# Optimization experiments

Hardware: AMD Instinct MI355X
Metric: run time of the kernel (lower is better)

## Reference

```python
import jax, jax.numpy as jnp
import numpy as np

D_MODEL = 1024
NUM_HEADS = 16
HEAD_DIM = D_MODEL // NUM_HEADS  # 64
D_FF = 4096
EPS = 1e-5


def layer_norm(x, gamma, beta):
    mu = jnp.mean(x, axis=-1, keepdims=True)
    var = jnp.mean((x - mu) ** 2, axis=-1, keepdims=True)
    return (x - mu) * jax.lax.rsqrt(var + EPS) * gamma + beta


def apply_rope(t):
    # t: [B, H, S, head_dim]; interleaved-pair rotation as in RoPE.apply_rope
    S, d = t.shape[-2], t.shape[-1]
    inv_freq = 1.0 / (10000.0 ** (jnp.arange(0, d, 2, dtype=jnp.float32) / d))  # [d/2]
    angles = jnp.arange(S, dtype=jnp.float32)[:, None] * inv_freq[None, :]      # [S, d/2]
    sin, cos = jnp.sin(angles), jnp.cos(angles)
    tp = t.reshape(*t.shape[:-1], d // 2, 2)  # pairs of adjacent elements
    t0, t1 = tp[..., 0], tp[..., 1]
    rot = jnp.stack([t0 * cos - t1 * sin, t0 * sin + t1 * cos], axis=-1)
    return rot.reshape(t.shape)


def setup_inputs() -> dict:
    key = jax.random.key(0)
    ks = jax.random.split(key, 18)
    s = 0.02
    d, f = D_MODEL, D_FF
    return {
        "x": jax.random.normal(ks[0], (2, 2048, d), dtype=jnp.float32),
        "Wq": jax.random.normal(ks[1], (d, d), dtype=jnp.float32) * s,
        "bq": jnp.zeros((d,), jnp.float32),
        "Wk": jax.random.normal(ks[2], (d, d), dtype=jnp.float32) * s,
        "bk": jnp.zeros((d,), jnp.float32),
        "Wv": jax.random.normal(ks[3], (d, d), dtype=jnp.float32) * s,
        "bv": jnp.zeros((d,), jnp.float32),
        "Wo": jax.random.normal(ks[4], (d, d), dtype=jnp.float32) * s,
        "bo": jnp.zeros((d,), jnp.float32),
        "W1": jax.random.normal(ks[5], (d, f), dtype=jnp.float32) * s,
        "b1": jnp.zeros((f,), jnp.float32),
        "W2": jax.random.normal(ks[6], (f, d), dtype=jnp.float32) * s,
        "b2": jnp.zeros((d,), jnp.float32),
        "g1": jnp.ones((d,), jnp.float32),
        "beta1": jnp.zeros((d,), jnp.float32),
        "g2": jnp.ones((d,), jnp.float32),
        "beta2": jnp.zeros((d,), jnp.float32),
    }


def reference(x, Wq, bq, Wk, bk, Wv, bv, Wo, bo, W1, b1, W2, b2, g1, beta1, g2, beta2):
    B, S, d = x.shape
    H, hd = NUM_HEADS, HEAD_DIM
    x_norm = layer_norm(x, g1, beta1)
    q = (x_norm @ Wq + bq).reshape(B, S, H, hd).transpose(0, 2, 1, 3)  # [B,H,S,hd]
    k = (x_norm @ Wk + bk).reshape(B, S, H, hd).transpose(0, 2, 1, 3)
    v = (x_norm @ Wv + bv).reshape(B, S, H, hd).transpose(0, 2, 1, 3)
    q = apply_rope(q)
    k = apply_rope(k)
    q = q * (1.0 / jnp.sqrt(jnp.float32(hd)))
    scores = jnp.einsum("bhqd,bhkd->bhqk", q, k)  # [B,H,S,S]
    attn = jax.nn.softmax(scores, axis=-1)
    out = jnp.einsum("bhqk,bhkd->bhqd", attn, v)
    out = out.transpose(0, 2, 1, 3).reshape(B, S, d)
    attn_out = out @ Wo + bo
    x = x + attn_out  # dropout p=0 (eval)
    x_norm2 = layer_norm(x, g2, beta2)
    ffn = jax.nn.relu(x_norm2 @ W1 + b1) @ W2 + b2
    return x + ffn
```

## Files before the change

### kernel.cpp

```cpp
#include <hip/hip_runtime.h>

typedef unsigned short bf16_t;
typedef short short8 __attribute__((ext_vector_type(8)));
typedef float f32x4 __attribute__((ext_vector_type(4)));
typedef float f32x16 __attribute__((ext_vector_type(16)));
typedef unsigned int u32x4 __attribute__((ext_vector_type(4)));

static __device__ __forceinline__ unsigned short f2bf(float f) {
  unsigned int u = __float_as_uint(f);
  unsigned int r = (u + 0x7FFFu + ((u >> 16) & 1u)) >> 16;
  return (unsigned short)r;
}
static __device__ __forceinline__ float bf2f(unsigned short u) {
  return __uint_as_float((unsigned int)u << 16);
}
static __device__ __forceinline__ unsigned int cvt_pk_bf16(float lo, float hi) {
  unsigned int r;
  asm("v_cvt_pk_bf16_f32 %0, %1, %2" : "=v"(r) : "v"(lo), "v"(hi));
  return r;
}
static __device__ __forceinline__ void pl32swap(unsigned int& a, unsigned int& b) {
  asm("v_permlane32_swap_b32 %0, %1" : "+v"(a), "+v"(b));
}

__device__ __forceinline__ void gload_lds16(const void* g, void* l) {
  __builtin_amdgcn_global_load_lds((const __attribute__((address_space(1))) void*)g,
                                   (__attribute__((address_space(3))) void*)l,
                                   16, 0, 0);
}

__global__ __launch_bounds__(256) void prep_kernel(
    const float* __restrict__ Wq, const float* __restrict__ Wk,
    const float* __restrict__ Wv, const float* __restrict__ Wo,
    const float* __restrict__ W1, const float* __restrict__ W2,
    const float* __restrict__ x, const float* __restrict__ g1,
    const float* __restrict__ be1,
    bf16_t* __restrict__ WqkvT, bf16_t* __restrict__ W1T,
    bf16_t* __restrict__ W2T, bf16_t* __restrict__ xnb) {
  __shared__ float tile[32][33];
  const int bid = blockIdx.x;
  if (bid < 12288) {
    const float* src;
    bf16_t* dst;
    int rows, cols, bx, by;
    if (bid < 4096) {
      const int z = bid >> 10, r = bid & 1023;
      src = (z == 0) ? Wq : (z == 1) ? Wk : (z == 2) ? Wv : Wo;
      dst = WqkvT + (size_t)z * 1048576;
      rows = 1024; cols = 1024;
      bx = (r & 31) * 32; by = (r >> 5) * 32;
    } else if (bid < 8192) {
      const int r = bid - 4096;
      src = W1; dst = W1T; rows = 1024; cols = 4096;
      bx = (r & 127) * 32; by = (r >> 7) * 32;
    } else {
      const int r = bid - 8192;
      src = W2; dst = W2T; rows = 4096; cols = 1024;
      bx = (r & 31) * 32; by = (r >> 5) * 32;
    }
    const int tx = threadIdx.x & 31, ty = threadIdx.x >> 5;
#pragma unroll
    for (int i = 0; i < 32; i += 8)
      tile[ty + i][tx] = src[(size_t)(by + ty + i) * cols + (bx + tx)];
    __syncthreads();
#pragma unroll
    for (int i = 0; i < 32; i += 8)
      dst[(size_t)(bx + ty + i) * rows + (by + tx)] = f2bf(tile[tx][ty + i]);
  } else {
    const int row = bid - 12288;
    const int tid = threadIdx.x;
    const float4 v = reinterpret_cast<const float4*>(x + (size_t)row * 1024)[tid];
    float s = v.x + v.y + v.z + v.w;
    float ss = v.x * v.x + v.y * v.y + v.z * v.z + v.w * v.w;
#pragma unroll
    for (int off = 32; off; off >>= 1) {
      s += __shfl_xor(s, off, 64);
      ss += __shfl_xor(ss, off, 64);
    }
    float* red = &tile[0][0];
    const int wave = tid >> 6, lane = tid & 63;
    if (lane == 0) { red[wave] = s; red[4 + wave] = ss; }
    __syncthreads();
    const float mu = (red[0] + red[1] + red[2] + red[3]) * (1.f / 1024.f);
    const float ms = (red[4] + red[5] + red[6] + red[7]) * (1.f / 1024.f);
    const float rstd = rsqrtf(ms - mu * mu + 1e-5f);
    const float4 gg = reinterpret_cast<const float4*>(g1)[tid];
    const float4 bb = reinterpret_cast<const float4*>(be1)[tid];
    bf16_t* o = xnb + (size_t)row * 1024 + tid * 4;
    o[0] = f2bf((v.x - mu) * rstd * gg.x + bb.x);
    o[1] = f2bf((v.y - mu) * rstd * gg.y + bb.y);
    o[2] = f2bf((v.z - mu) * rstd * gg.z + bb.z);
    o[3] = f2bf((v.w - mu) * rstd * gg.w + bb.w);
  }
}

__global__ __launch_bounds__(256) void ln2_combine(const bf16_t* __restrict__ p,
                                                   const float* __restrict__ x,
                                                   const float* __restrict__ bo,
                                                   const float* __restrict__ g,
                                                   const float* __restrict__ be,
                                                   float* __restrict__ x2,
                                                   bf16_t* __restrict__ xn) {
  const int row = blockIdx.x;
  const int tid = threadIdx.x;
  const float4 xv = reinterpret_cast<const float4*>(x + (size_t)row * 1024)[tid];
  const float4 bb = reinterpret_cast<const float4*>(bo)[tid];
  float4 v = {bb.x + xv.x, bb.y + xv.y, bb.z + xv.z, bb.w + xv.w};
#pragma unroll
  for (int z = 0; z < 4; ++z) {
    const ushort4 a = reinterpret_cast<const ushort4*>(p + (size_t)z * 4194304 + (size_t)row * 1024)[tid];
    v.x += bf2f(a.x); v.y += bf2f(a.y); v.z += bf2f(a.z); v.w += bf2f(a.w);
  }
  reinterpret_cast<float4*>(x2 + (size_t)row * 1024)[tid] = v;
  float s = v.x + v.y + v.z + v.w;
  float ss = v.x * v.x + v.y * v.y + v.z * v.z + v.w * v.w;
#pragma unroll
  for (int off = 32; off; off >>= 1) {
    s += __shfl_xor(s, off, 64);
    ss += __shfl_xor(ss, off, 64);
  }
  __shared__ float red[8];
  const int wave = tid >> 6, lane = tid & 63;
  if (lane == 0) { red[wave] = s; red[4 + wave] = ss; }
  __syncthreads();
  const float mu = (red[0] + red[1] + red[2] + red[3]) * (1.f / 1024.f);
  const float ms = (red[4] + red[5] + red[6] + red[7]) * (1.f / 1024.f);
  const float rstd = rsqrtf(ms - mu * mu + 1e-5f);
  const float4 gg = reinterpret_cast<const float4*>(g)[tid];
  const float4 eb = reinterpret_cast<const float4*>(be)[tid];
  bf16_t* o = xn + (size_t)row * 1024 + tid * 4;
  o[0] = f2bf((v.x - mu) * rstd * gg.x + eb.x);
  o[1] = f2bf((v.y - mu) * rstd * gg.y + eb.y);
  o[2] = f2bf((v.z - mu) * rstd * gg.z + eb.z);
  o[3] = f2bf((v.w - mu) * rstd * gg.w + eb.w);
}

__global__ __launch_bounds__(256) void ffn_combine(const bf16_t* __restrict__ p0,
                                                   const bf16_t* __restrict__ p2,
                                                   const float* __restrict__ x2,
                                                   const float* __restrict__ b2,
                                                   float* __restrict__ out) {
  const int row = blockIdx.x;
  const int tid = threadIdx.x;
  const ushort4 a0 = reinterpret_cast<const ushort4*>(p0 + (size_t)row * 1024)[tid];
  const ushort4 a1 = reinterpret_cast<const ushort4*>(p0 + 4194304 + (size_t)row * 1024)[tid];
  const ushort4 a2 = reinterpret_cast<const ushort4*>(p2 + (size_t)row * 1024)[tid];
  const float4 xv = reinterpret_cast<const float4*>(x2 + (size_t)row * 1024)[tid];
  const float4 bb = reinterpret_cast<const float4*>(b2)[tid];
  float4 v;
  v.x = bf2f(a0.x) + bf2f(a1.x) + bf2f(a2.x) + bb.x + xv.x;
  v.y = bf2f(a0.y) + bf2f(a1.y) + bf2f(a2.y) + bb.y + xv.y;
  v.z = bf2f(a0.z) + bf2f(a1.z) + bf2f(a2.z) + bb.z + xv.z;
  v.w = bf2f(a0.w) + bf2f(a1.w) + bf2f(a2.w) + bb.w + xv.w;
  reinterpret_cast<float4*>(out + (size_t)row * 1024)[tid] = v;
}

__global__ __launch_bounds__(256) void rope_bf16(bf16_t* __restrict__ q,
                                                 bf16_t* __restrict__ k) {
  const int id = blockIdx.x * 256 + threadIdx.x;
  const int i = id & 31;
  const int s = (id >> 5) & 2047;
  const int bh = id >> 16;
  const float inv = exp2f((float)i * -0.41524101186f);
  float sn, cs;
  sincosf((float)s * inv, &sn, &cs);
  const size_t base = ((size_t)bh * 2048 + s) * 64 + 2 * i;
  unsigned int qp = *(unsigned int*)&q[base];
  unsigned int kp = *(unsigned int*)&k[base];
  const float q0 = bf2f(qp & 0xffff), q1 = bf2f(qp >> 16);
  const float k0 = bf2f(kp & 0xffff), k1 = bf2f(kp >> 16);
  const float qs = 0.18033688f;
  const unsigned int qo =
      (unsigned int)f2bf((q0 * cs - q1 * sn) * qs) |
      ((unsigned int)f2bf((q0 * sn + q1 * cs) * qs) << 16);
  const unsigned int ko =
      (unsigned int)f2bf(k0 * cs - k1 * sn) |
      ((unsigned int)f2bf(k0 * sn + k1 * cs) << 16);
  *(unsigned int*)&q[base] = qo;
  *(unsigned int*)&k[base] = ko;
}

__global__ __launch_bounds__(256) void vtrans(const bf16_t* __restrict__ v,
                                              bf16_t* __restrict__ vt) {
  __shared__ bf16_t tile[32][33];
  const int bh = blockIdx.x;
  const int s0 = blockIdx.y * 32;
  const int d0 = blockIdx.z * 32;
  const int tx = threadIdx.x & 31, ty = threadIdx.x >> 5;
  const size_t base = (size_t)bh * (2048 * 64);
#pragma unroll
  for (int i = 0; i < 32; i += 8)
    tile[ty + i][tx] = v[base + (size_t)(s0 + ty + i) * 64 + d0 + tx];
  __syncthreads();
#pragma unroll
  for (int i = 0; i < 32; i += 8)
    vt[base + (size_t)(d0 + ty + i) * 2048 + s0 + tx] = tile[tx][ty + i];
}

__global__ __launch_bounds__(256, 2) void attn6(const bf16_t* __restrict__ qb,
                                                const bf16_t* __restrict__ kb,
                                                const bf16_t* __restrict__ vt,
                                                bf16_t* __restrict__ out) {
  const int bh = blockIdx.x;
  const int tid = threadIdx.x, wave = tid >> 6, lane = tid & 63;
  const int l31 = lane & 31, hi = lane >> 5;
  const int q0 = blockIdx.y * 128 + wave * 32;
  const size_t kvb = (size_t)bh * (2048 * 64);

  __shared__ __align__(16) bf16_t Ks[2][2][4096];
  __shared__ __align__(16) bf16_t Vs[2][2][4096];

  short8 qf[4];
#pragma unroll
  for (int st = 0; st < 4; ++st)
    qf[st] = *(const short8*)&qb[kvb + (size_t)(q0 + l31) * 64 + st * 16 + hi * 8];

  int kidx[2][4];
  int vidx[2][2][2];
#pragma unroll
  for (int st = 0; st < 4; ++st) {
    const int R0 = l31, R1 = 32 + l31;
    kidx[0][st] = (R0 * 8 + (((st << 1) | hi) ^ (R0 & 7))) * 8;
    kidx[1][st] = (R1 * 8 + (((st << 1) | hi) ^ (R1 & 7))) * 8;
  }
#pragma unroll
  for (int f = 0; f < 2; ++f)
#pragma unroll
    for (int ks = 0; ks < 2; ++ks) {
      const int R0 = l31, R1 = 32 + l31;
      vidx[0][f][ks] = (R0 * 8 + (((f << 2) | (ks << 1) | hi) ^ (R0 & 7))) * 8;
      vidx[1][f][ks] = (R1 * 8 + (((f << 2) | (ks << 1) | hi) ^ (R1 & 7))) * 8;
    }

  short8 vones;
#pragma unroll
  for (int j = 0; j < 8; ++j) vones[j] = (short)0x3F80;

  f32x16 acc0 = {}, acc1 = {}, lacc = {};
  const f32x16 fz = {};

#define STAGE(DST, T0)                                                                     \
  {                                                                                        \
    _Pragma("unroll") for (int sub = 0; sub < 2; ++sub) {                                  \
      _Pragma("unroll") for (int j = 0; j < 2; ++j) {                                      \
        const int s = wave * 128 + j * 64 + lane;                                          \
        const int r = s >> 3;                                                              \
        const int c = (s & 7) ^ (r & 7);                                                   \
        gload_lds16(kb + kvb + (size_t)((T0) + sub * 64 + r) * 64 + c * 8,                 \
                    &Ks[DST][sub][(size_t)s * 8]);                                         \
        gload_lds16(vt + kvb + (size_t)r * 2048 + (T0) + sub * 64 + c * 8,                 \
                    &Vs[DST][sub][(size_t)s * 8]);                                         \
      }                                                                                    \
    }                                                                                      \
  }

#define QK(BUF, SUB, P0, P1)                                                               \
  {                                                                                        \
    short8 kfa[4], kfb[4];                                                                 \
    _Pragma("unroll") for (int st = 0; st < 4; ++st) {                                     \
      kfa[st] = *(const short8*)&Ks[BUF][SUB][kidx[0][st]];                                \
      kfb[st] = *(const short8*)&Ks[BUF][SUB][kidx[1][st]];                                \
    }                                                                                      \
    __builtin_amdgcn_s_setprio(1);                                                         \
    P0 = __builtin_amdgcn_mfma_f32_32x32x16_bf16(kfa[0], qf[0], fz, 0, 0, 0);              \
    P1 = __builtin_amdgcn_mfma_f32_32x32x16_bf16(kfb[0], qf[0], fz, 0, 0, 0);              \
    _Pragma("unroll") for (int st = 1; st < 4; ++st) {                                     \
      P0 = __builtin_amdgcn_mfma_f32_32x32x16_bf16(kfa[st], qf[st], P0, 0, 0, 0);          \
      P1 = __builtin_amdgcn_mfma_f32_32x32x16_bf16(kfb[st], qf[st], P1, 0, 0, 0);          \
    }                                                                                      \
    __builtin_amdgcn_s_setprio(0);                                                         \
  }

#define SMPV(BUF, SUB, P0, P1)                                                             \
  {                                                                                        \
    _Pragma("unroll") for (int f = 0; f < 2; ++f) {                                        \
      f32x16& p = f ? P1 : P0;                                                             \
      float e[16];                                                                         \
      _Pragma("unroll") for (int r = 0; r < 16; ++r) e[r] = exp2f(p[r]);                   \
      unsigned int a0 = cvt_pk_bf16(e[0], e[1]), b0 = cvt_pk_bf16(e[4], e[5]);             \
      unsigned int a1 = cvt_pk_bf16(e[2], e[3]), b1 = cvt_pk_bf16(e[6], e[7]);             \
      unsigned int a2 = cvt_pk_bf16(e[8], e[9]), b2 = cvt_pk_bf16(e[12], e[13]);           \
      unsigned int a3 = cvt_pk_bf16(e[10], e[11]), b3 = cvt_pk_bf16(e[14], e[15]);         \
      pl32swap(a0, b0);                                                                    \
      pl32swap(a1, b1);                                                                    \
      pl32swap(a2, b2);                                                                    \
      pl32swap(a3, b3);                                                                    \
      const u32x4 w0 = {a0, a1, b0, b1};                                                   \
      const u32x4 w1 = {a2, a3, b2, b3};                                                   \
      const short8 pf0 = __builtin_bit_cast(short8, w0);                                   \
      const short8 pf1 = __builtin_bit_cast(short8, w1);                                   \
      const short8 vf00 = *(const short8*)&Vs[BUF][SUB][vidx[0][f][0]];                    \
      const short8 vf10 = *(const short8*)&Vs[BUF][SUB][vidx[1][f][0]];                    \
      const short8 vf01 = *(const short8*)&Vs[BUF][SUB][vidx[0][f][1]];                    \
      const short8 vf11 = *(const short8*)&Vs[BUF][SUB][vidx[1][f][1]];                    \
      __builtin_amdgcn_s_setprio(1);                                                       \
      lacc = __builtin_amdgcn_mfma_f32_32x32x16_bf16(pf0, vones, lacc, 0, 0, 0);           \
      acc0 = __builtin_amdgcn_mfma_f32_32x32x16_bf16(pf0, vf00, acc0, 0, 0, 0);            \
      acc1 = __builtin_amdgcn_mfma_f32_32x32x16_bf16(pf0, vf10, acc1, 0, 0, 0);            \
      lacc = __builtin_amdgcn_mfma_f32_32x32x16_bf16(pf1, vones, lacc, 0, 0, 0);           \
      acc0 = __builtin_amdgcn_mfma_f32_32x32x16_bf16(pf1, vf01, acc0, 0, 0, 0);            \
      acc1 = __builtin_amdgcn_mfma_f32_32x32x16_bf16(pf1, vf11, acc1, 0, 0, 0);            \
      __builtin_amdgcn_s_setprio(0);                                                       \
    }                                                                                      \
  }

#define CITER(BUF, NT0, DOPREF)                                                            \
  {                                                                                        \
    if (DOPREF) {                                                                          \
      STAGE((BUF) ^ 1, NT0);                                                               \
      asm volatile("s_waitcnt vmcnt(8)" ::: "memory");                                     \
    } else {                                                                               \
      asm volatile("s_waitcnt vmcnt(0)" ::: "memory");                                     \
    }                                                                                      \
    __builtin_amdgcn_s_barrier();                                                          \
    asm volatile("" ::: "memory");                                                         \
    f32x16 pa0, pa1, pb0, pb1;                                                             \
    QK(BUF, 0, pa0, pa1);                                                                  \
    QK(BUF, 1, pb0, pb1);                                                                  \
    SMPV(BUF, 0, pa0, pa1);                                                                \
    SMPV(BUF, 1, pb0, pb1);                                                                \
    asm volatile("" ::: "memory");                                                         \
    __builtin_amdgcn_s_barrier();                                                          \
    asm volatile("" ::: "memory");                                                         \
  }

  STAGE(0, 0);

  for (int k = 0; k < 7; ++k) {
    CITER(0, (2 * k + 1) * 128, 1)
    CITER(1, (2 * k + 2) * 128, 1)
  }
  CITER(0, 1920, 1)
  CITER(1, 0, 0)
#undef CITER
#undef SMPV
#undef QK
#undef STAGE

  const int b = bh >> 4, h = bh & 15;
#pragma unroll
  for (int r = 0; r < 16; ++r) {
    const int qrow = (r & 3) + 8 * (r >> 2) + 4 * hi;
    const float rl = 1.f / lacc[r];
    const size_t ro = (size_t)(b * 2048 + q0 + qrow) * 1024 + h * 64;
    out[ro + l31] = f2bf(acc0[r] * rl);
    out[ro + 32 + l31] = f2bf(acc1[r] * rl);
  }
}

enum { MODE_QKV = 0, MODE_FF1 = 1, MODE_PART = 2 };

template <int MODE>
__global__ __launch_bounds__(256) void gemm_bt(
    const bf16_t* __restrict__ A, const bf16_t* __restrict__ BT,
    int M, int N, int K, int kspan,
    const float* __restrict__ bias0, const float* __restrict__ bias1,
    const float* __restrict__ bias2,
    bf16_t* __restrict__ ob0, bf16_t* __restrict__ ob1, bf16_t* __restrict__ ob2) {
  __shared__ __align__(16) char smem[34816];
  bf16_t* As = (bf16_t*)smem;
  bf16_t* Bs = (bf16_t*)(smem + 16384);
  const int tid = threadIdx.x;
  const int wave = tid >> 6, lane = tid & 63;
  const int row16 = lane & 15, quad = lane >> 4;
  const int m0 = blockIdx.x * 128, n0 = blockIdx.y * 128;
  const int wm = (wave & 1) << 6, wn = (wave >> 1) << 6;

  f32x4 acc[4][4];
#pragma unroll
  for (int i = 0; i < 4; ++i)
#pragma unroll
    for (int j = 0; j < 4; ++j) acc[i][j] = (f32x4){0.f, 0.f, 0.f, 0.f};

  const int kb = blockIdx.z * kspan;
  const int kend = (kb + kspan < K) ? kb + kspan : K;

  for (int k0 = kb; k0 < kend; k0 += 64) {
#pragma unroll
    for (int j = 0; j < 4; ++j) {
      const int s = j * 256 + tid;
      const int r = s >> 3;
      const int cg = ((s & 7) ^ (r & 7)) << 3;
      gload_lds16(A + (size_t)(m0 + r) * K + k0 + cg, As + (size_t)s * 8);
      gload_lds16(BT + (size_t)(n0 + r) * K + k0 + cg, Bs + (size_t)s * 8);
    }
    __syncthreads();
    const int sw = row16 & 7;
#pragma unroll
    for (int kk = 0; kk < 2; ++kk) {
      short8 af[4], bfr[4];
#pragma unroll
      for (int mi = 0; mi < 4; ++mi)
        af[mi] = *(const short8*)&As[(size_t)(wm + mi * 16 + row16) * 64 + (((kk << 2) | quad) ^ sw) * 8];
#pragma unroll
      for (int ni = 0; ni < 4; ++ni)
        bfr[ni] = *(const short8*)&Bs[(size_t)(wn + ni * 16 + row16) * 64 + (((kk << 2) | quad) ^ sw) * 8];
#pragma unroll
      for (int mi = 0; mi < 4; ++mi)
#pragma unroll
        for (int ni = 0; ni < 4; ++ni)
          acc[mi][ni] =
              __builtin_amdgcn_mfma_f32_16x16x32_bf16(af[mi], bfr[ni], acc[mi][ni], 0, 0, 0);
    }
    __syncthreads();
  }

  bf16_t* ct = (bf16_t*)smem;
#pragma unroll
  for (int mi = 0; mi < 4; ++mi)
#pragma unroll
    for (int ni = 0; ni < 4; ++ni) {
      const int gn = n0 + wn + ni * 16 + row16;
      float bsv = 0.f;
      if (MODE == MODE_QKV)
        bsv = (gn < 1024) ? bias0[gn] : (gn < 2048) ? bias1[gn - 1024] : bias2[gn - 2048];
      else if (MODE == MODE_FF1)
        bsv = bias0[gn];
#pragma unroll
      for (int r = 0; r < 4; ++r) {
        float c = acc[mi][ni][r] + bsv;
        if (MODE == MODE_FF1) c = fmaxf(c, 0.f);
        ct[(size_t)(wm + mi * 16 + quad * 4 + r) * 136 + wn + ni * 16 + row16] = f2bf(c);
      }
    }
  __syncthreads();
  const int lr0 = tid >> 4, lc = tid & 15;
#pragma unroll
  for (int i = 0; i < 8; ++i) {
    const int lr = i * 16 + lr0;
    const uint4 v = *(const uint4*)&ct[(size_t)lr * 136 + lc * 8];
    const int gm = m0 + lr;
    if (MODE == MODE_QKV) {
      const int nn = (n0 & 1023) + lc * 8;
      const int h = nn >> 6, d = nn & 63;
      const int b = gm >> 11, s = gm & 2047;
      bf16_t* dst = (n0 < 1024) ? ob0 : (n0 < 2048) ? ob1 : ob2;
      *(uint4*)&dst[(((size_t)b * 16 + h) * 2048 + s) * 64 + d] = v;
    } else if (MODE == MODE_FF1) {
      *(uint4*)&ob0[(size_t)gm * N + n0 + lc * 8] = v;
    } else {
      bf16_t* dst = (blockIdx.z == 2) ? ob1 : ob0 + (size_t)blockIdx.z * 4194304;
      *(uint4*)&dst[(size_t)gm * N + n0 + lc * 8] = v;
    }
  }
}

extern "C" void kernel_launch(void* const* d_in, const int* in_sizes, int n_in,
                              void* d_out, int out_size, void* d_ws, size_t ws_size,
                              hipStream_t stream) {
  const float* x = (const float*)d_in[0];
  const float* Wq = (const float*)d_in[1];
  const float* bq = (const float*)d_in[2];
  const float* Wk = (const float*)d_in[3];
  const float* bk = (const float*)d_in[4];
  const float* Wv = (const float*)d_in[5];
  const float* bv = (const float*)d_in[6];
  const float* Wo = (const float*)d_in[7];
  const float* bo = (const float*)d_in[8];
  const float* W1 = (const float*)d_in[9];
  const float* b1 = (const float*)d_in[10];
  const float* W2 = (const float*)d_in[11];
  const float* b2 = (const float*)d_in[12];
  const float* g1 = (const float*)d_in[13];
  const float* be1 = (const float*)d_in[14];
  const float* g2 = (const float*)d_in[15];
  const float* be2 = (const float*)d_in[16];
  float* out = (float*)d_out;

  char* ws = (char*)d_ws;
  size_t off = 0;
  auto alloc = [&](size_t bytes) {
    void* p = ws + off;
    off += (bytes + 255) & ~(size_t)255;
    return p;
  };
  bf16_t* WqkvT = (bf16_t*)alloc(3072ULL * 1024 * 2);
  bf16_t* WoT = (bf16_t*)alloc(1024ULL * 1024 * 2);
  bf16_t* W1T = (bf16_t*)alloc(4096ULL * 1024 * 2);
  bf16_t* W2T = (bf16_t*)alloc(1024ULL * 4096 * 2);
  bf16_t* xnb = (bf16_t*)alloc(4096ULL * 1024 * 2);
  bf16_t* qb = (bf16_t*)alloc(4194304ULL * 2);
  bf16_t* kb = (bf16_t*)alloc(4194304ULL * 2);
  bf16_t* vraw = (bf16_t*)alloc(4194304ULL * 2);
  bf16_t* vt = (bf16_t*)alloc(4194304ULL * 2);
  bf16_t* h1 = qb;
  bf16_t* x2p = qb;
  bf16_t* ffp = WqkvT;
  float* x2 = (float*)alloc(16777216ULL);

  prep_kernel<<<16384, 256, 0, stream>>>(Wq, Wk, Wv, Wo, W1, W2, x, g1, be1,
                                         WqkvT, W1T, W2T, xnb);

  gemm_bt<MODE_QKV><<<dim3(32, 24, 1), 256, 0, stream>>>(xnb, WqkvT, 4096, 3072, 1024, 1024,
                                                         bq, bk, bv, qb, kb, vraw);

  rope_bf16<<<8192, 256, 0, stream>>>(qb, kb);

  vtrans<<<dim3(32, 64, 2), 256, 0, stream>>>(vraw, vt);

  attn6<<<dim3(32, 16), 256, 0, stream>>>(qb, kb, vt, xnb);

  gemm_bt<MODE_PART><<<dim3(32, 8, 4), 256, 0, stream>>>(xnb, WoT, 4096, 1024, 1024, 256,
                                                         nullptr, nullptr, nullptr,
                                                         x2p, x2p + 2 * 4194304, nullptr);

  ln2_combine<<<4096, 256, 0, stream>>>(x2p, x, bo, g2, be2, x2, xnb);

  gemm_bt<MODE_FF1><<<dim3(32, 32, 1), 256, 0, stream>>>(xnb, W1T, 4096, 4096, 1024, 1024,
                                                         b1, nullptr, nullptr,
                                                         h1, nullptr, nullptr);

  gemm_bt<MODE_PART><<<dim3(32, 8, 3), 256, 0, stream>>>(h1, W2T, 4096, 1024, 4096, 1408,
                                                         nullptr, nullptr, nullptr,
                                                         ffp, xnb, nullptr);

  ffn_combine<<<4096, 256, 0, stream>>>(ffp, xnb, x2, b2, out);
}
```

Baseline: 364.7 us.

## Add 256x256 pipelined FF1 GEMM kernel and use native exp2 in attention

Replaces the 128x128 FF1 GEMM with a dedicated 512-thread kernel that uses 256x256 tiles, 128KB of dynamic LDS, swizzled async global-to-LDS staging and a phased double-buffered schedule with explicit vmcnt waits. The fused bias+ReLU epilogue goes through LDS for coalesced stores. The aim is more operand reuse per tile and better overlap of loads with MFMA. Separately, attention switches exp2f to native exp2, dropping the range-handling code at a small accuracy cost. The large LDS footprint limits occupancy, and with 256 blocks the grid may underfill the CUs.

```diff
diff --git a/kernel.cpp b/kernel.cpp
--- a/kernel.cpp
+++ b/kernel.cpp
@@ -5,6 +5,8 @@
 typedef float f32x4 __attribute__((ext_vector_type(4)));
 typedef float f32x16 __attribute__((ext_vector_type(16)));
 typedef unsigned int u32x4 __attribute__((ext_vector_type(4)));
+
+extern "C" __device__ float __ocml_native_exp2_f32(float);
 
 static __device__ __forceinline__ unsigned short f2bf(float f) {
   unsigned int u = __float_as_uint(f);
@@ -197,7 +199,7 @@
     vt[base + (size_t)(d0 + ty + i) * 2048 + s0 + tx] = tile[tx][ty + i];
 }
 
-__global__ __launch_bounds__(256, 2) void attn6(const bf16_t* __restrict__ qb,
+__global__ __launch_bounds__(256, 2) void attn7(const bf16_t* __restrict__ qb,
                                                 const bf16_t* __restrict__ kb,
                                                 const bf16_t* __restrict__ vt,
                                                 bf16_t* __restrict__ out) {
@@ -276,7 +278,7 @@
     _Pragma("unroll") for (int f = 0; f < 2; ++f) {                                        \
       f32x16& p = f ? P1 : P0;                                                             \
       float e[16];                                                                         \
-      _Pragma("unroll") for (int r = 0; r < 16; ++r) e[r] = exp2f(p[r]);                   \
+      _Pragma("unroll") for (int r = 0; r < 16; ++r) e[r] = __ocml_native_exp2_f32(p[r]);  \
       unsigned int a0 = cvt_pk_bf16(e[0], e[1]), b0 = cvt_pk_bf16(e[4], e[5]);             \
       unsigned int a1 = cvt_pk_bf16(e[2], e[3]), b1 = cvt_pk_bf16(e[6], e[7]);             \
       unsigned int a2 = cvt_pk_bf16(e[8], e[9]), b2 = cvt_pk_bf16(e[12], e[13]);           \
@@ -348,6 +350,133 @@
   }
 }
 
+#define SWZ4(r) (((r) ^ ((r) >> 2)) & 3)
+#define HP(SL, H) (dynlds + (size_t)(((SL) * 4 + (H)) * 8192))
+
+#define STAGE8(dst, src, row0, kc0)                                             \
+  {                                                                             \
+    _Pragma("unroll") for (int j = 0; j < 2; ++j) {                             \
+      const int s_ = j * 512 + tid;                                             \
+      const int r_ = s_ >> 2;                                                   \
+      const int c_ = (s_ & 3) ^ SWZ4(r_);                                       \
+      gload_lds16(src + (size_t)((row0) + r_) * 1024 + (kc0) + c_ * 8,          \
+                  (dst) + (size_t)s_ * 8);                                      \
+    }                                                                           \
+  }
+
+#define PHASE(SL, KH, MH, STG, VMW)                                             \
+  {                                                                             \
+    STG;                                                                        \
+    short8 af_[4];                                                              \
+    _Pragma("unroll") for (int q4 = 0; q4 < 4; ++q4)                            \
+      af_[q4] = *(const short8*)(HP(SL, KH) + aidx[(MH) * 4 + q4]);             \
+    if ((MH) == 0) {                                                            \
+      _Pragma("unroll") for (int ni = 0; ni < 4; ++ni)                          \
+        bfr[ni] = *(const short8*)(HP(SL, 2 + (KH)) + bidx[ni]);                \
+    }                                                                           \
+    VMW;                                                                        \
+    asm volatile("" ::: "memory");                                              \
+    __builtin_amdgcn_s_barrier();                                               \
+    asm volatile("" ::: "memory");                                              \
+    __builtin_amdgcn_s_setprio(1);                                              \
+    _Pragma("unroll") for (int q4 = 0; q4 < 4; ++q4)                            \
+      _Pragma("unroll") for (int ni = 0; ni < 4; ++ni)                          \
+        acc[(MH) * 4 + q4][ni] = __builtin_amdgcn_mfma_f32_16x16x32_bf16(       \
+            af_[q4], bfr[ni], acc[(MH) * 4 + q4][ni], 0, 0, 0);                 \
+    __builtin_amdgcn_s_setprio(0);                                              \
+    asm volatile("" ::: "memory");                                              \
+    __builtin_amdgcn_s_barrier();                                               \
+    asm volatile("" ::: "memory");                                              \
+  }
+
+#define KTILE(SL, KT, VM2, VM4)                                                 \
+  PHASE(SL, 0, 0,                                                               \
+        if ((KT) + 1 < 16) STAGE8(HP((SL) ^ 1, 2), BT, n0, ((KT) + 1) * 64),    \
+        (void)0)                                                                \
+  PHASE(SL, 0, 1,                                                               \
+        if ((KT) + 1 < 16) STAGE8(HP((SL) ^ 1, 1), A, m0, ((KT) + 1) * 64 + 32),\
+        asm volatile("s_waitcnt vmcnt(" #VM2 ")" ::: "memory"))                 \
+  PHASE(SL, 1, 0,                                                               \
+        if ((KT) + 1 < 16) STAGE8(HP((SL) ^ 1, 3), BT, n0, ((KT) + 1) * 64 + 32),\
+        (void)0)                                                                \
+  PHASE(SL, 1, 1,                                                               \
+        if ((KT) + 2 < 16) STAGE8(HP(SL, 0), A, m0, ((KT) + 2) * 64),           \
+        asm volatile("s_waitcnt vmcnt(" #VM4 ")" ::: "memory"))
+
+__global__ __launch_bounds__(512, 2) void gemm_ff1_256(
+    const bf16_t* __restrict__ A, const bf16_t* __restrict__ BT,
+    const float* __restrict__ bias, bf16_t* __restrict__ ob) {
+  extern __shared__ bf16_t dynlds[];
+  const int tid = threadIdx.x;
+  const int wave = tid >> 6, lane = tid & 63;
+  const int row16 = lane & 15, quad = lane >> 4;
+  const int wr = wave >> 2, wc = wave & 3;
+  const int m0 = blockIdx.x * 256, n0 = blockIdx.y * 256;
+
+  int aidx[8], bidx[4];
+#pragma unroll
+  for (int mi = 0; mi < 8; ++mi) {
+    const int R = wr * 128 + mi * 16 + row16;
+    aidx[mi] = R * 32 + (quad ^ SWZ4(R)) * 8;
+  }
+#pragma unroll
+  for (int ni = 0; ni < 4; ++ni) {
+    const int R = wc * 64 + ni * 16 + row16;
+    bidx[ni] = R * 32 + (quad ^ SWZ4(R)) * 8;
+  }
+
+  f32x4 acc[8][4];
+#pragma unroll
+  for (int i = 0; i < 8; ++i)
+#pragma unroll
+    for (int j = 0; j < 4; ++j) acc[i][j] = (f32x4){0.f, 0.f, 0.f, 0.f};
+  short8 bfr[4];
+
+  STAGE8(HP(0, 0), A, m0, 0);
+  STAGE8(HP(0, 2), BT, n0, 0);
+  STAGE8(HP(0, 1), A, m0, 32);
+  STAGE8(HP(0, 3), BT, n0, 32);
+  STAGE8(HP(1, 0), A, m0, 64);
+  __syncthreads();
+
+  for (int kt2 = 0; kt2 < 7; ++kt2) {
+    const int kt = 2 * kt2;
+    KTILE(0, kt, 6, 4)
+    KTILE(1, kt + 1, 6, 4)
+  }
+  KTILE(0, 14, 6, 4)
+  KTILE(1, 15, 0, 0)
+
+  __syncthreads();
+  bf16_t* ct = dynlds;
+  float bsv[4];
+#pragma unroll
+  for (int ni = 0; ni < 4; ++ni) bsv[ni] = bias[n0 + wc * 64 + ni * 16 + row16];
+#pragma unroll
+  for (int mh = 0; mh < 2; ++mh) {
+    if (wr == mh) {
+#pragma unroll
+      for (int mi = 0; mi < 8; ++mi)
+#pragma unroll
+        for (int ni = 0; ni < 4; ++ni)
+#pragma unroll
+          for (int r = 0; r < 4; ++r) {
+            const float c = fmaxf(acc[mi][ni][r] + bsv[ni], 0.f);
+            ct[(size_t)(mi * 16 + quad * 4 + r) * 264 + wc * 64 + ni * 16 + row16] = f2bf(c);
+          }
+    }
+    __syncthreads();
+#pragma unroll
+    for (int it = 0; it < 8; ++it) {
+      const int u = it * 512 + tid;
+      const int lr = u >> 5, lcq = u & 31;
+      const uint4 v = *(const uint4*)&ct[(size_t)lr * 264 + lcq * 8];
+      *(uint4*)&ob[(size_t)(m0 + mh * 128 + lr) * 4096 + n0 + lcq * 8] = v;
+    }
+    __syncthreads();
+  }
+}
+
 enum { MODE_QKV = 0, MODE_FF1 = 1, MODE_PART = 2 };
 
 template <int MODE>
@@ -488,6 +617,13 @@
   bf16_t* ffp = WqkvT;
   float* x2 = (float*)alloc(16777216ULL);
 
+  static bool attrset = false;
+  if (!attrset) {
+    hipFuncSetAttribute((const void*)gemm_ff1_256,
+                        hipFuncAttributeMaxDynamicSharedMemorySize, 131072);
+    attrset = true;
+  }
+
   prep_kernel<<<16384, 256, 0, stream>>>(Wq, Wk, Wv, Wo, W1, W2, x, g1, be1,
                                          WqkvT, W1T, W2T, xnb);
 
@@ -498,7 +634,7 @@
 
   vtrans<<<dim3(32, 64, 2), 256, 0, stream>>>(vraw, vt);
 
-  attn6<<<dim3(32, 16), 256, 0, stream>>>(qb, kb, vt, xnb);
+  attn7<<<dim3(32, 16), 256, 0, stream>>>(qb, kb, vt, xnb);
 
   gemm_bt<MODE_PART><<<dim3(32, 8, 4), 256, 0, stream>>>(xnb, WoT, 4096, 1024, 1024, 256,
                                                          nullptr, nullptr, nullptr,
@@ -506,9 +642,7 @@
 
   ln2_combine<<<4096, 256, 0, stream>>>(x2p, x, bo, g2, be2, x2, xnb);
 
-  gemm_bt<MODE_FF1><<<dim3(32, 32, 1), 256, 0, stream>>>(xnb, W1T, 4096, 4096, 1024, 1024,
-                                                         b1, nullptr, nullptr,
-                                                         h1, nullptr, nullptr);
+  gemm_ff1_256<<<dim3(16, 16), 512, 131072, stream>>>(xnb, W1T, b1, h1);
 
   gemm_bt<MODE_PART><<<dim3(32, 8, 3), 256, 0, stream>>>(h1, W2T, 4096, 1024, 4096, 1408,
                                                          nullptr, nullptr, nullptr,
```

Measured after the change: 344.7 us. 5.5% less time.
